# Kernel tuning notes

Hardware: AMD Instinct MI355X
Metric: run time of the kernel (lower is better)

Reference implementation:

```python
import jax, jax.numpy as jnp
import numpy as np

N = 8192        # agents (single node type VEHICLE)
K = 15          # max_Nnode - 1 neighbors per node
E = N * K       # edges
FT = 12         # prediction horizon steps
SD = 4          # state dim (x, y, vx, vy)
ID = 2          # input dim (ax, ay)
ZD = 8          # latent z dim
HE = 256        # history_enc_dim
EE = 128        # edge_enc_dim
OH = 256        # obs_lstm_hidden_dim
GH = 256        # guide_RNN_hidden_dim
FH = 256        # FC_hidden_dim
AD = 16         # att_internal_dim
DT = 0.25
SCALE = 1.0     # input_scale


def setup_inputs() -> dict:
    ks = jax.random.split(jax.random.key(0), 40)
    f = lambda i, s: jax.random.normal(ks[i], s, jnp.float32)
    w = lambda i, s: 0.05 * jax.random.normal(ks[i], s, jnp.float32)
    inp = dict(
        x_last=f(0, (N, SD)), x_st_last=f(1, (N, SD)), hist_enc=f(2, (N, HE)),
        z=f(3, (N, ZD)),
        node_size=jax.random.uniform(ks[4], (N, 2), jnp.float32, 1.0, 3.0),
        W_h0=w(5, (SD, OH)), b_h0=w(6, (OH,)), W_c0=w(7, (SD, OH)), b_c0=w(8, (OH,)),
        W_gh=w(9, (HE + ZD, GH)), b_gh=w(10, (GH,)),
        W_gru_ih=w(11, (HE + ZD, 3 * GH)), W_gru_hh=w(12, (GH, 3 * GH)),
        b_gru_ih=w(13, (3 * GH,)), b_gru_hh=w(14, (3 * GH,)),
        W_proj=w(15, (GH, 2)), b_proj=w(16, (2,)),
        W_att1=w(17, (EE, AD)), W_att2=w(18, (SD, AD)), v_att=w(19, (AD,)),
        W_lstm_ih=w(20, (EE, 4 * OH)), W_lstm_hh=w(21, (OH, 4 * OH)),
        b_lstm_ih=w(22, (4 * OH,)), b_lstm_hh=w(23, (4 * OH,)),
        W_e1=w(24, (SD + 4, FH)), b_e1=w(25, (FH,)), W_e2=w(26, (FH, EE)), b_e2=w(27, (EE,)),
        W_a1=w(28, (OH + ZD + SD + 4, FH)), b_a1=w(29, (FH,)),
        W_a2=w(30, (FH, ID)), b_a2=w(31, (ID,)),
    )
    # edge k is the j-th neighbor of node k // K; index 0 in the enc table is the pad row
    inp["edge_idx1"] = jnp.repeat(jnp.arange(N), K)
    inp["edge_idx2"] = jax.random.randint(ks[32], (E,), 0, N)
    inp["node_obs_idx"] = (jnp.arange(E) + 1).reshape(N, K)
    inp["ft"] = FT
    return inp


def _dyn(s, u):
    # double-integrator: s = [x, y, vx, vy], u = [ax, ay]
    pos = s[:, :2] + s[:, 2:4] * DT + 0.5 * u * DT * DT
    vel = s[:, 2:4] + u * DT
    return jnp.concatenate([pos, vel], -1)


def _forward(x_last, x_st_last, hist_enc, z, node_size,
             W_h0, b_h0, W_c0, b_c0, W_gh, b_gh, W_gru_ih, W_gru_hh, b_gru_ih, b_gru_hh,
             W_proj, b_proj, W_att1, W_att2, v_att, W_lstm_ih, W_lstm_hh, b_lstm_ih, b_lstm_hh,
             W_e1, b_e1, W_e2, b_e2, W_a1, b_a1, W_a2, b_a2,
             edge_idx1, edge_idx2, node_obs_idx, ft):
    n = x_last.shape[0]
    ee = W_e2.shape[1]
    # ---- guide GRU: desired trajectory [ft, N, 2] ----
    xz = jnp.concatenate([hist_enc, z], -1)
    h0g = xz @ W_gh + b_gh
    gi = xz @ W_gru_ih + b_gru_ih  # input is constant over time (xz repeated)
    ir, iz, inn = jnp.split(gi, 3, -1)

    def gru_step(h, _):
        hr, hz, hn = jnp.split(h @ W_gru_hh + b_gru_hh, 3, -1)
        r = jax.nn.sigmoid(ir + hr)
        u = jax.nn.sigmoid(iz + hz)
        nh = (1.0 - u) * jnp.tanh(inn + r * hn) + u * h
        return nh, nh

    _, hs = jax.lax.scan(gru_step, h0g, None, length=ft)
    des = hs @ W_proj + b_proj                       # [ft, N, 2]
    des_next = jnp.concatenate([des[1:], des[-1:]], 0)
    des_prev = jnp.concatenate([jnp.zeros_like(des[:1]), des[:-1]], 0)
    first = jnp.zeros((ft,), jnp.float32).at[0].set(1.0)

    # ---- obs LSTM initial state ----
    h0 = x_st_last @ W_h0 + b_h0
    c0 = x_st_last @ W_c0 + b_c0

    size1 = node_size[edge_idx1]
    size2 = node_size[edge_idx2]
    rad = 0.5 * (jnp.linalg.norm(size1, axis=-1) + jnp.linalg.norm(size2, axis=-1))

    def step(carry, xs):
        prev, prev_st, h, c, terr, ccost = carry
        des_t, des_n, des_p, fst = xs
        # edge gather + collision cost + edge encoding
        s1 = prev[edge_idx1]
        s2 = prev[edge_idx2]
        dist = jnp.linalg.norm(s1[:, :2] - s2[:, :2], axis=-1)
        ccost = ccost + jnp.sum(jax.nn.relu(rad - dist))
        feat = jnp.concatenate([s2 - s1, size1, size2], -1)          # [E, SD+4]
        enc = jax.nn.relu(feat @ W_e1 + b_e1) @ W_e2 + b_e2          # [E, EE]
        enc_all = jnp.concatenate([jnp.zeros((1, ee), enc.dtype), enc], 0)
        obs = enc_all[node_obs_idx]                                   # [N, K, EE]
        # relative state (t==0 uses standardized history directly)
        m = 1.0 - fst
        rel = prev_st - m * x_st_last
        rel = jnp.concatenate([rel[:, :2] - m * des_p, rel[:, 2:]], -1)
        terr = terr + jnp.linalg.norm(rel[:, :2]) / n
        next_wp = des_t - prev_st[:, :2]
        next_wp2 = des_n - prev_st[:, :2]
        # additive attention over neighbors
        scores = jnp.tanh(obs @ W_att1 + (rel @ W_att2)[:, None, :]) @ v_att   # [N, K]
        att = jax.nn.softmax(scores, axis=-1)
        ctx = jnp.einsum('nk,nkd->nd', att, obs)
        # LSTM cell (torch gate order i, f, g, o)
        gates = ctx @ W_lstm_ih + b_lstm_ih + h @ W_lstm_hh + b_lstm_hh
        g_i, g_f, g_g, g_o = jnp.split(gates, 4, -1)
        c = jax.nn.sigmoid(g_f) * c + jax.nn.sigmoid(g_i) * jnp.tanh(g_g)
        h = jax.nn.sigmoid(g_o) * jnp.tanh(c)
        # action net + dynamics rollout
        a_in = jnp.concatenate([h, z, rel, next_wp, next_wp2], -1)   # [N, OH+ZD+SD+4]
        u = SCALE * jnp.tanh(jax.nn.relu(a_in @ W_a1 + b_a1) @ W_a2 + b_a2)
        nxt = _dyn(prev, u)
        nxt_st = _dyn(prev_st, u)
        return (nxt, nxt_st, h, c, terr, ccost), (nxt, u)

    zero = jnp.zeros((), jnp.float32)
    init = (x_last, x_st_last, h0, c0, zero, zero)
    (_, _, _, _, terr, ccost), (state_pred, input_pred) = jax.lax.scan(
        step, init, (des, des_next, des_prev, first))
    return state_pred, input_pred, terr, ccost


def reference(x_last, x_st_last, hist_enc, z, node_size,
              W_h0, b_h0, W_c0, b_c0, W_gh, b_gh, W_gru_ih, W_gru_hh, b_gru_ih, b_gru_hh,
              W_proj, b_proj, W_att1, W_att2, v_att, W_lstm_ih, W_lstm_hh, b_lstm_ih, b_lstm_hh,
              W_e1, b_e1, W_e2, b_e2, W_a1, b_a1, W_a2, b_a2,
              edge_idx1, edge_idx2, node_obs_idx, ft):
    return _forward(x_last, x_st_last, hist_enc, z, node_size,
                    W_h0, b_h0, W_c0, b_c0, W_gh, b_gh, W_gru_ih, W_gru_hh, b_gru_ih, b_gru_hh,
                    W_proj, b_proj, W_att1, W_att2, v_att, W_lstm_ih, W_lstm_hh, b_lstm_ih, b_lstm_hh,
                    W_e1, b_e1, W_e2, b_e2, W_a1, b_a1, W_a2, b_a2,
                    edge_idx1, edge_idx2, node_obs_idx, ft)
```

## Files before the change

### kernel.cpp

```cpp
#include <hip/hip_runtime.h>

#define DEVI __device__ __forceinline__

constexpr int N_  = 8192;
constexpr int K_  = 15;
constexpr int E_  = N_ * K_;
constexpr int FTS = 12;
constexpr float DT_ = 0.25f;

typedef __attribute__((ext_vector_type(8))) short short8x;
typedef __attribute__((ext_vector_type(4))) float float4x;

union U8 { unsigned int u[4]; short8x v; };

DEVI float sigf(float x) { return 1.0f / (1.0f + __expf(-x)); }
DEVI float tanhf_fast(float x) { float e = __expf(2.f * x); return 1.f - 2.f / (e + 1.f); }
DEVI unsigned int f2u(float x) { union { float f; unsigned int u; } c; c.f = x; return c.u; }
DEVI float u2f(unsigned int x) { union { unsigned int u; float f; } c; c.u = x; return c.f; }

DEVI void split8(const float* __restrict__ s, short8x& hi8, short8x& lo8) {
  U8 ph, pl;
#pragma unroll
  for (int p = 0; p < 4; p++) {
    float a0 = s[2*p], a1 = s[2*p+1];
    unsigned int u0 = f2u(a0), u1 = f2u(a1);
    unsigned int h0 = u0 & 0xFFFF0000u, h1 = u1 & 0xFFFF0000u;
    ph.u[p] = (u0 >> 16) | h1;
    float l0 = a0 - u2f(h0), l1 = a1 - u2f(h1);
    pl.u[p] = (f2u(l0) >> 16) | (f2u(l1) & 0xFFFF0000u);
  }
  hi8 = ph.v; lo8 = pl.v;
}

__global__ void k_zero(float* ss) {
  ss[blockIdx.x * 256 + threadIdx.x] = 0.f;
}

__global__ __launch_bounds__(256) void k_edge_static(
    const int* __restrict__ e1, const int* __restrict__ e2,
    const float* __restrict__ nsize, float* __restrict__ rad, float* __restrict__ szf)
{
  int e = blockIdx.x * 256 + threadIdx.x;
  if (e >= E_) return;
  int i1 = e1[e], i2 = e2[e];
  float s1x = nsize[i1*2+0], s1y = nsize[i1*2+1];
  float s2x = nsize[i2*2+0], s2y = nsize[i2*2+1];
  rad[e] = 0.5f * (sqrtf(s1x*s1x + s1y*s1y) + sqrtf(s2x*s2x + s2y*s2y));
  *(float4*)&szf[e*4] = make_float4(s1x, s1y, s2x, s2y);
}

__global__ __launch_bounds__(256) void k_prep_hi(
    const float* __restrict__ W, unsigned short* __restrict__ out)
{
  int t = blockIdx.x * 256 + threadIdx.x;
  int fid = t >> 6, L = t & 63;
  int ks = fid >> 3, nt = fid & 7;
  int k0 = ks * 32 + (L >> 4) * 8;
  int n  = nt * 16 + (L & 15);
  unsigned int hi[4];
#pragma unroll
  for (int p = 0; p < 4; p++) {
    float w0 = W[(size_t)(k0 + 2*p) * 128 + n];
    float w1 = W[(size_t)(k0 + 2*p + 1) * 128 + n];
    hi[p] = (f2u(w0) >> 16) | (f2u(w1) & 0xFFFF0000u);
  }
  *(uint4*)(out + (size_t)fid * 512 + (size_t)L * 8) = make_uint4(hi[0], hi[1], hi[2], hi[3]);
}

__global__ __launch_bounds__(256) void k_prep1(
    const float* __restrict__ WA, const float* __restrict__ WB,
    int mode, int split, int wA, int wB, int Ktot, int NT, int nfrag,
    unsigned short* __restrict__ out)
{
  int t = blockIdx.x * 256 + threadIdx.x;
  int fid = t >> 6, L = t & 63;
  if (fid >= nfrag) return;
  int ks = fid / NT, nt = fid % NT;
  int k0 = ks * 32 + (L >> 4) * 8;
  int n  = nt * 16 + (L & 15);
  unsigned int hi[4];
#pragma unroll
  for (int p = 0; p < 4; p++) {
    float w0 = 0.f, w1 = 0.f;
    int ka = k0 + 2*p, kb = ka + 1;
    if (mode == 0) {
      if (ka < Ktot) w0 = (ka < split) ? WA[(size_t)ka*wA + n] : WB[(size_t)(ka-split)*wB + n];
      if (kb < Ktot) w1 = (kb < split) ? WA[(size_t)kb*wA + n] : WB[(size_t)(kb-split)*wB + n];
    } else {
      if (ka < Ktot) w0 = (n < split) ? WA[(size_t)ka*wA + n] : WB[(size_t)ka*wB + (n-split)];
      if (kb < Ktot) w1 = (n < split) ? WA[(size_t)kb*wA + n] : WB[(size_t)kb*wB + (n-split)];
    }
    hi[p] = (f2u(w0) >> 16) | (f2u(w1) & 0xFFFF0000u);
  }
  *(uint4*)(out + (size_t)fid * 512 + (size_t)L * 8) = make_uint4(hi[0], hi[1], hi[2], hi[3]);
}

__global__ __launch_bounds__(256) void k_xz_mfma(
    const float* __restrict__ hist, const float* __restrict__ z,
    const unsigned short* __restrict__ wB,
    const float* __restrict__ b_gh, const float* __restrict__ b_gih,
    float* __restrict__ gh0, unsigned int* __restrict__ gi_ru,
    float* __restrict__ gi_n)
{
  __shared__ __align__(16) float Abuf[2][64][36];
  const int tid = threadIdx.x;
  const int w = tid >> 6, lane = tid & 63;
  const int m = lane & 15, q = lane >> 4;
  const int n0 = blockIdx.x * 64;
  const int r_ = tid >> 2, c_ = (tid & 3) * 8;
  float4x acc[16];
#pragma unroll
  for (int tl = 0; tl < 16; tl++) acc[tl] = (float4x){0.f,0.f,0.f,0.f};

  auto LD = [&](int ks, float4& v0, float4& v1) {
    int kk = ks*32 + c_;
    int n = n0 + r_;
    if (kk < 256) {
      v0 = *(const float4*)&hist[(size_t)n*256 + kk];
      v1 = *(const float4*)&hist[(size_t)n*256 + kk + 4];
    } else if (kk == 256) {
      v0 = *(const float4*)&z[n*8];
      v1 = *(const float4*)&z[n*8 + 4];
    } else {
      v0 = make_float4(0,0,0,0); v1 = v0;
    }
  };
  {
    float4 v0, v1; LD(0, v0, v1);
    *(float4*)&Abuf[0][r_][c_]     = v0;
    *(float4*)&Abuf[0][r_][c_ + 4] = v1;
  }
  __syncthreads();
  for (int ks = 0; ks < 9; ks++) {
    float4 v0, v1;
    if (ks < 8) LD(ks + 1, v0, v1);
    short8x aHi, aLo;
    split8(&Abuf[ks & 1][w*16 + m][q*8], aHi, aLo);
#pragma unroll
    for (int tl = 0; tl < 16; tl++) {
      int nt = blockIdx.y*16 + tl;
      size_t off = (size_t)(ks*64 + nt) * 512 + (size_t)lane*8;
      short8x bh = *(const short8x*)(wB + off);
      acc[tl] = __builtin_amdgcn_mfma_f32_16x16x32_bf16(aLo, bh, acc[tl], 0, 0, 0);
      acc[tl] = __builtin_amdgcn_mfma_f32_16x16x32_bf16(aHi, bh, acc[tl], 0, 0, 0);
    }
    if (ks < 8) {
      *(float4*)&Abuf[(ks+1) & 1][r_][c_]     = v0;
      *(float4*)&Abuf[(ks+1) & 1][r_][c_ + 4] = v1;
      __syncthreads();
    }
  }
#pragma unroll
  for (int tl = 0; tl < 16; tl++) {
    int col = (blockIdx.y*16 + tl)*16 + m;
    float bias = (col < 256) ? b_gh[col] : b_gih[col - 256];
#pragma unroll
    for (int i = 0; i < 4; i++) {
      int n = n0 + w*16 + q*4 + i;
      float v = acc[tl][i] + bias;
      if (col < 256) {
        gh0[(size_t)n*256 + col] = v;
      } else {
        int cj = col - 256;
        int gate = cj >> 8, j = cj & 255;
        if (gate == 2) gi_n[(size_t)n*256 + j] = v;
        else ((unsigned short*)gi_ru)[((size_t)n*256 + j)*2 + gate] =
               (unsigned short)(f2u(v) >> 16);
      }
    }
  }
}

__global__ __launch_bounds__(512) void k_gru_all(
    const float* __restrict__ gh0, const unsigned short* __restrict__ wB,
    const float* __restrict__ b_ghh,
    const unsigned int* __restrict__ gi_ru, const float* __restrict__ gi_n,
    const float* __restrict__ W_proj, const float* __restrict__ b_proj,
    float* __restrict__ des)
{
  __shared__ __align__(16) float h_lds[2][32][260];
  __shared__ float sm_des[4][32][2];
  const int tid = threadIdx.x;
  const int w = tid >> 6, lane = tid & 63;
  const int m = lane & 15, q = lane >> 4;
  const int rh = w & 1, jh = w >> 1;
  const int n0 = blockIdx.x * 32;

  {
    int r = tid >> 4, c = (tid & 15) * 16;
    const float4* src = (const float4*)&gh0[(size_t)(n0 + r)*256 + c];
    float4 v0 = src[0], v1 = src[1], v2 = src[2], v3 = src[3];
    *(float4*)&h_lds[0][r][c]      = v0;
    *(float4*)&h_lds[0][r][c + 4]  = v1;
    *(float4*)&h_lds[0][r][c + 8]  = v2;
    *(float4*)&h_lds[0][r][c + 12] = v3;
  }
  float br_[4], bz_[4], bn_[4], wp0_[4], wp1_[4];
#pragma unroll
  for (int jt = 0; jt < 4; jt++) {
    int j = jh*64 + jt*16 + m;
    br_[jt] = b_ghh[j];
    bz_[jt] = b_ghh[256 + j];
    bn_[jt] = b_ghh[512 + j];
    wp0_[jt] = W_proj[j*2];
    wp1_[jt] = W_proj[j*2 + 1];
  }
  const float bp0 = b_proj[0], bp1 = b_proj[1];
  __syncthreads();

  for (int t = 0; t < FTS; t++) {
    float (*hc)[260] = h_lds[t & 1];
    float (*hn)[260] = h_lds[(t + 1) & 1];
    float4x acc[12];
#pragma unroll
    for (int tl = 0; tl < 12; tl++) acc[tl] = (float4x){0.f,0.f,0.f,0.f};

#pragma unroll 2
    for (int ks = 0; ks < 8; ks++) {
      float a8[8];
      {
        const float* hp = &hc[rh*16 + m][ks*32 + q*8];
        float4 v0 = *(const float4*)hp;
        float4 v1 = *(const float4*)(hp + 4);
        a8[0]=v0.x; a8[1]=v0.y; a8[2]=v0.z; a8[3]=v0.w;
        a8[4]=v1.x; a8[5]=v1.y; a8[6]=v1.z; a8[7]=v1.w;
      }
      short8x aHi, aLo;
      split8(a8, aHi, aLo);
#pragma unroll
      for (int tl = 0; tl < 12; tl++) {
        int g = tl >> 2, jt = tl & 3;
        int nt = g*16 + jh*4 + jt;
        size_t off = (size_t)(ks*48 + nt) * 512 + (size_t)lane*8;
        short8x bh = *(const short8x*)(wB + off);
        acc[tl] = __builtin_amdgcn_mfma_f32_16x16x32_bf16(aLo, bh, acc[tl], 0, 0, 0);
        acc[tl] = __builtin_amdgcn_mfma_f32_16x16x32_bf16(aHi, bh, acc[tl], 0, 0, 0);
      }
    }
    float pd0[4] = {0,0,0,0}, pd1[4] = {0,0,0,0};
#pragma unroll
    for (int jt = 0; jt < 4; jt++) {
      int j = jh*64 + jt*16 + m;
#pragma unroll
      for (int i = 0; i < 4; i++) {
        int rl = rh*16 + q*4 + i;
        unsigned int ru = gi_ru[(size_t)(n0 + rl)*256 + j];
        float ir  = u2f(ru << 16);
        float iz  = u2f(ru & 0xFFFF0000u);
        float inn = gi_n[(size_t)(n0 + rl)*256 + j];
        float hold = hc[rl][j];
        float r = sigf(ir + acc[0*4 + jt][i] + br_[jt]);
        float u = sigf(iz + acc[1*4 + jt][i] + bz_[jt]);
        float nh = (1.f - u) * tanhf_fast(inn + r * (acc[2*4 + jt][i] + bn_[jt])) + u * hold;
        hn[rl][j] = nh;
        pd0[i] += nh * wp0_[jt];
        pd1[i] += nh * wp1_[jt];
      }
    }
#pragma unroll
    for (int off = 1; off < 16; off <<= 1) {
#pragma unroll
      for (int i = 0; i < 4; i++) {
        pd0[i] += __shfl_xor(pd0[i], off);
        pd1[i] += __shfl_xor(pd1[i], off);
      }
    }
    if (m == 0) {
#pragma unroll
      for (int i = 0; i < 4; i++) {
        sm_des[jh][rh*16 + q*4 + i][0] = pd0[i];
        sm_des[jh][rh*16 + q*4 + i][1] = pd1[i];
      }
    }
    __syncthreads();
    if (tid < 64) {
      int r = tid >> 1, c = tid & 1;
      float s = sm_des[0][r][c] + sm_des[1][r][c] + sm_des[2][r][c] + sm_des[3][r][c];
      des[((size_t)t * N_ + n0 + r) * 2 + c] = s + (c ? bp1 : bp0);
    }
    __syncthreads();
  }
}

__global__ __launch_bounds__(256) void k_lstm_mfma(
    const float* __restrict__ ctxg, const float* __restrict__ h_in,
    const unsigned short* __restrict__ wB,
    const float* __restrict__ b_ih, const float* __restrict__ b_hh,
    float* __restrict__ c_st, float* __restrict__ h_out)
{
  __shared__ __align__(16) float Abuf[2][64][36];
  const int tid = threadIdx.x;
  const int w = tid >> 6, lane = tid & 63;
  const int m = lane & 15, q = lane >> 4;
  const int n0 = blockIdx.x * 64;
  const int j0 = blockIdx.y * 32;
  const int r_ = tid >> 2, c_ = (tid & 3) * 8;
  float4x acc[8];
#pragma unroll
  for (int tl = 0; tl < 8; tl++) acc[tl] = (float4x){0.f,0.f,0.f,0.f};

  auto LD = [&](int ks, float4& v0, float4& v1) {
    int kk = ks*32 + c_;
    int n = n0 + r_;
    if (kk < 128) {
      v0 = *(const float4*)&ctxg[(size_t)n*128 + kk];
      v1 = *(const float4*)&ctxg[(size_t)n*128 + kk + 4];
    } else {
      v0 = *(const float4*)&h_in[(size_t)n*256 + kk - 128];
      v1 = *(const float4*)&h_in[(size_t)n*256 + kk - 124];
    }
  };
  {
    float4 v0, v1; LD(0, v0, v1);
    *(float4*)&Abuf[0][r_][c_]     = v0;
    *(float4*)&Abuf[0][r_][c_ + 4] = v1;
  }
  __syncthreads();
  for (int ks = 0; ks < 12; ks++) {
    float4 v0, v1;
    if (ks < 11) LD(ks + 1, v0, v1);
    short8x aHi, aLo;
    split8(&Abuf[ks & 1][w*16 + m][q*8], aHi, aLo);
#pragma unroll
    for (int tl = 0; tl < 8; tl++) {
      int g = tl >> 1, jt = tl & 1;
      int nt = g*16 + (j0 >> 4) + jt;
      size_t off = (size_t)(ks*64 + nt) * 512 + (size_t)lane*8;
      short8x bh = *(const short8x*)(wB + off);
      acc[tl] = __builtin_amdgcn_mfma_f32_16x16x32_bf16(aLo, bh, acc[tl], 0, 0, 0);
      acc[tl] = __builtin_amdgcn_mfma_f32_16x16x32_bf16(aHi, bh, acc[tl], 0, 0, 0);
    }
    if (ks < 11) {
      *(float4*)&Abuf[(ks+1) & 1][r_][c_]     = v0;
      *(float4*)&Abuf[(ks+1) & 1][r_][c_ + 4] = v1;
      __syncthreads();
    }
  }
#pragma unroll
  for (int jt = 0; jt < 2; jt++) {
    int j = j0 + jt*16 + m;
    float bi = b_ih[j]       + b_hh[j];
    float bf = b_ih[256 + j] + b_hh[256 + j];
    float bg = b_ih[512 + j] + b_hh[512 + j];
    float bo = b_ih[768 + j] + b_hh[768 + j];
#pragma unroll
    for (int i = 0; i < 4; i++) {
      int n = n0 + w*16 + q*4 + i;
      float g_i = sigf(acc[0*2 + jt][i] + bi);
      float g_f = sigf(acc[1*2 + jt][i] + bf);
      float g_g = tanhf_fast(acc[2*2 + jt][i] + bg);
      float g_o = sigf(acc[3*2 + jt][i] + bo);
      float cv = g_f * c_st[(size_t)n*256 + j] + g_i * g_g;
      c_st[(size_t)n*256 + j] = cv;
      h_out[(size_t)n*256 + j] = g_o * tanhf_fast(cv);
    }
  }
}

__global__ __launch_bounds__(256) void k_action_mfma(
    const float* __restrict__ h, const float* __restrict__ z,
    const float* __restrict__ rel, const float* __restrict__ nwp, const float* __restrict__ nwp2,
    const unsigned short* __restrict__ wB, const float* __restrict__ b_a1,
    const float* __restrict__ W_a2, const float* __restrict__ b_a2,
    float* __restrict__ prev, float* __restrict__ prev_st,
    float* __restrict__ outS, float* __restrict__ outU)
{
  __shared__ __align__(16) float Abuf[2][32][36];
  __shared__ float sm_p[2][16][2];
  const int tid = threadIdx.x;
  const int w = tid >> 6, lane = tid & 63;
  const int m = lane & 15, q = lane >> 4;
  const int ng = w >> 1, hh = w & 1;
  const int n0 = blockIdx.x * 32;
  const int r_ = tid >> 3, c_ = (tid & 7) * 4;
  float4x acc[8];
#pragma unroll
  for (int j = 0; j < 8; j++) acc[j] = (float4x){0.f,0.f,0.f,0.f};

  auto LD = [&](int ks) -> float4 {
    int kk = ks*32 + c_;
    int n = n0 + r_;
    float4 v;
    if (kk < 256)       v = *(const float4*)&h[(size_t)n*256 + kk];
    else if (kk == 256) v = *(const float4*)&z[n*8];
    else if (kk == 260) v = *(const float4*)&z[n*8 + 4];
    else if (kk == 264) v = *(const float4*)&rel[n*4];
    else if (kk == 268) {
      float2 w1 = *(const float2*)&nwp[n*2];
      float2 w2 = *(const float2*)&nwp2[n*2];
      v = make_float4(w1.x, w1.y, w2.x, w2.y);
    } else v = make_float4(0,0,0,0);
    return v;
  };
  {
    float4 v = LD(0);
    *(float4*)&Abuf[0][r_][c_] = v;
  }
  __syncthreads();
  for (int ks = 0; ks < 9; ks++) {
    float4 v;
    if (ks < 8) v = LD(ks + 1);
    short8x aHi, aLo;
    split8(&Abuf[ks & 1][ng*16 + m][q*8], aHi, aLo);
#pragma unroll
    for (int j = 0; j < 8; j++) {
      int tl = hh*8 + j;
      size_t off = (size_t)(ks*16 + tl) * 512 + (size_t)lane*8;
      short8x bh = *(const short8x*)(wB + off);
      acc[j] = __builtin_amdgcn_mfma_f32_16x16x32_bf16(aLo, bh, acc[j], 0, 0, 0);
      acc[j] = __builtin_amdgcn_mfma_f32_16x16x32_bf16(aHi, bh, acc[j], 0, 0, 0);
    }
    if (ks < 8) {
      *(float4*)&Abuf[(ks+1) & 1][r_][c_] = v;
      __syncthreads();
    }
  }
  float p0[4] = {0,0,0,0}, p1[4] = {0,0,0,0};
#pragma unroll
  for (int j = 0; j < 8; j++) {
    int col = (hh*8 + j)*16 + m;
    float ba = b_a1[col];
    float2 w2 = *(const float2*)&W_a2[col*2];
#pragma unroll
    for (int i = 0; i < 4; i++) {
      float hv = fmaxf(acc[j][i] + ba, 0.f);
      p0[i] += hv * w2.x;
      p1[i] += hv * w2.y;
    }
  }
#pragma unroll
  for (int off = 1; off < 16; off <<= 1) {
#pragma unroll
    for (int i = 0; i < 4; i++) {
      p0[i] += __shfl_xor(p0[i], off);
      p1[i] += __shfl_xor(p1[i], off);
    }
  }
  if (hh == 1 && m == 0) {
#pragma unroll
    for (int i = 0; i < 4; i++) {
      sm_p[ng][q*4 + i][0] = p0[i];
      sm_p[ng][q*4 + i][1] = p1[i];
    }
  }
  __syncthreads();
  if (hh == 0 && m == 0) {
    float ba0 = b_a2[0], ba1 = b_a2[1];
    const float hd = 0.5f * DT_ * DT_;
#pragma unroll
    for (int i = 0; i < 4; i++) {
      int n = n0 + ng*16 + q*4 + i;
      float ux = tanhf_fast(p0[i] + sm_p[ng][q*4 + i][0] + ba0);
      float uy = tanhf_fast(p1[i] + sm_p[ng][q*4 + i][1] + ba1);
      float4 pv = *(const float4*)&prev[n*4];
      float4 ps = *(const float4*)&prev_st[n*4];
      float4 npv, nps;
      npv.x = pv.x + pv.z*DT_ + ux*hd;
      npv.y = pv.y + pv.w*DT_ + uy*hd;
      npv.z = pv.z + ux*DT_;
      npv.w = pv.w + uy*DT_;
      nps.x = ps.x + ps.z*DT_ + ux*hd;
      nps.y = ps.y + ps.w*DT_ + uy*hd;
      nps.z = ps.z + ux*DT_;
      nps.w = ps.w + uy*DT_;
      *(float4*)&prev[n*4] = npv;
      *(float4*)&prev_st[n*4] = nps;
      *(float4*)&outS[(size_t)n*4] = npv;
      outU[n*2]     = ux;
      outU[n*2 + 1] = uy;
    }
  }
}

__global__ __launch_bounds__(256) void k_init_hc(
    const float* __restrict__ x_last, const float* __restrict__ x_st_last,
    const float* __restrict__ W_h0, const float* __restrict__ b_h0,
    const float* __restrict__ W_c0, const float* __restrict__ b_c0,
    float* __restrict__ h, float* __restrict__ c,
    float* __restrict__ prev, float* __restrict__ prev_st)
{
  const int n = blockIdx.x;
  const int j = threadIdx.x;
  float x0 = x_st_last[n*4], x1 = x_st_last[n*4+1], x2 = x_st_last[n*4+2], x3 = x_st_last[n*4+3];
  h[(size_t)n*256 + j] = b_h0[j] + x0*W_h0[j] + x1*W_h0[256+j] + x2*W_h0[512+j] + x3*W_h0[768+j];
  c[(size_t)n*256 + j] = b_c0[j] + x0*W_c0[j] + x1*W_c0[256+j] + x2*W_c0[512+j] + x3*W_c0[768+j];
  if (j < 4) prev[n*4 + j] = x_last[n*4 + j];
  else if (j < 8) prev_st[n*4 + (j-4)] = x_st_last[n*4 + (j-4)];
}

__global__ __launch_bounds__(256, 4) void k_edge(
    const float* __restrict__ prev, const float* __restrict__ prev_st,
    const float* __restrict__ x_st_last,
    const float* __restrict__ szf, const float* __restrict__ rad,
    const int* __restrict__ nobs, const int* __restrict__ e1, const int* __restrict__ e2,
    const float* __restrict__ W_e1, const float* __restrict__ b_e1,
    const unsigned short* __restrict__ wsB, const float* __restrict__ b_e2,
    const unsigned short* __restrict__ wattA, const float* __restrict__ W_att2,
    const float* __restrict__ v_att,
    const float* __restrict__ des_p, const float* __restrict__ des_t,
    const float* __restrict__ des_n,
    float* __restrict__ relg, float* __restrict__ nwp, float* __restrict__ nwp2,
    float* __restrict__ ctx, float* __restrict__ ss_t, float* __restrict__ cc)
{
  __shared__ __align__(16) float smem[4776];
  const int tid = threadIdx.x;
  const int eb = blockIdx.x;

  float* sm_stage = smem;
  float* sm_feats = smem + 4096;
  float* sm_flags = smem + 4608;
  float* sm_relv  = smem + 4672;
  float* sm_watt2 = smem + 4688;
  float* sm_vatt  = smem + 4752;
  float* sm_red   = smem + 4768;

  const int n0  = eb * 4;
  const int slot = (eb & 15) << 4;
  const int lane = tid & 63;
  const int g    = tid >> 6;
  const int q = lane >> 4, m = lane & 15;

  if (tid >= 176 && tid < 192) sm_vatt[tid - 176] = v_att[tid - 176];
  if (tid >= 192) sm_watt2[tid - 192] = W_att2[tid - 192];

  if (tid < 64) {
    float v = 0.f;
    if (tid < 60) {
      int gg = tid / 15, k = tid % 15;
      int idx = nobs[(n0 + gg) * 15 + k];
      float f[8] = {0,0,0,0,0,0,0,0};
      float fl = 0.f;
      if (idx > 0) {
        int e = idx - 1;
        int i1 = e1[e], i2 = e2[e];
#pragma unroll
        for (int d = 0; d < 4; d++) f[d] = prev[i2*4 + d] - prev[i1*4 + d];
        float4 sz = *(const float4*)&szf[(size_t)e*4];
        f[4] = sz.x; f[5] = sz.y; f[6] = sz.z; f[7] = sz.w;
        fl = 1.f;
        float dist = sqrtf(f[0]*f[0] + f[1]*f[1]);
        v = fmaxf(rad[e] - dist, 0.f);
      }
#pragma unroll
      for (int d = 0; d < 8; d++) sm_feats[(gg*16 + k)*8 + d] = f[d];
      sm_flags[gg*16 + k] = fl;
    } else {
      int gg = tid - 60;
#pragma unroll
      for (int d = 0; d < 8; d++) sm_feats[(gg*16 + 15)*8 + d] = 0.f;
      sm_flags[gg*16 + 15] = 0.f;
    }
#pragma unroll
    for (int off = 32; off; off >>= 1) v += __shfl_down(v, off);
    if (tid == 0) atomicAdd(cc + slot, v);
  } else if (tid < 68) {
    int gg = tid - 64;
    int n = n0 + gg;
    float4 ps = *(const float4*)&prev_st[n*4];
    float r0, r1, r2, r3;
    if (des_p) {
      float4 xs = *(const float4*)&x_st_last[n*4];
      r0 = ps.x - xs.x - des_p[n*2];
      r1 = ps.y - xs.y - des_p[n*2 + 1];
      r2 = ps.z - xs.z;
      r3 = ps.w - xs.w;
    } else { r0 = ps.x; r1 = ps.y; r2 = ps.z; r3 = ps.w; }
    sm_relv[gg*4+0] = r0; sm_relv[gg*4+1] = r1; sm_relv[gg*4+2] = r2; sm_relv[gg*4+3] = r3;
    *(float4*)&relg[n*4] = make_float4(r0, r1, r2, r3);
    nwp[n*2]      = des_t[n*2]     - ps.x;
    nwp[n*2 + 1]  = des_t[n*2 + 1] - ps.y;
    nwp2[n*2]     = des_n[n*2]     - ps.x;
    nwp2[n*2 + 1] = des_n[n*2 + 1] - ps.y;
    sm_red[gg] = r0*r0 + r1*r1;
  }
  {
    const uint4* src = (const uint4*)wsB;
    uint4* dst = (uint4*)sm_stage;
    dst[tid]       = src[tid];
    dst[tid + 256] = src[tid + 256];
  }
  __syncthreads();
  if (tid == 64) atomicAdd(ss_t + slot, sm_red[0] + sm_red[1] + sm_red[2] + sm_red[3]);

  float f[8];
  {
    const float4 fa = *(const float4*)&sm_feats[(g*16 + m)*8];
    const float4 fb = *(const float4*)&sm_feats[(g*16 + m)*8 + 4];
    f[0]=fa.x; f[1]=fa.y; f[2]=fa.z; f[3]=fa.w; f[4]=fb.x; f[5]=fb.y; f[6]=fb.z; f[7]=fb.w;
  }
  float4x encR[8];
#pragma unroll
  for (int nt = 0; nt < 8; nt++) encR[nt] = (float4x){0.f,0.f,0.f,0.f};
  const float4* We14 = (const float4*)W_e1;
  const float4* Be14 = (const float4*)b_e1;

  for (int ks = 0; ks < 8; ks++) {
    uint4 r0, r1;
    if (ks < 7) {
      const uint4* src = (const uint4*)wsB + (ks + 1) * 512;
      r0 = src[tid];
      r1 = src[tid + 256];
    }
    short8x aHi, aLo;
    {
      float h8[8];
      float4 b0 = Be14[8*ks + 2*q];
      float4 b1 = Be14[8*ks + 2*q + 1];
      h8[0]=b0.x; h8[1]=b0.y; h8[2]=b0.z; h8[3]=b0.w; h8[4]=b1.x; h8[5]=b1.y; h8[6]=b1.z; h8[7]=b1.w;
#pragma unroll
      for (int d = 0; d < 8; d++) {
        float4 wa = We14[d*64 + ks*8 + 2*q];
        float4 wb = We14[d*64 + ks*8 + 2*q + 1];
        h8[0] += f[d]*wa.x; h8[1] += f[d]*wa.y; h8[2] += f[d]*wa.z; h8[3] += f[d]*wa.w;
        h8[4] += f[d]*wb.x; h8[5] += f[d]*wb.y; h8[6] += f[d]*wb.z; h8[7] += f[d]*wb.w;
      }
#pragma unroll
      for (int p = 0; p < 8; p++) h8[p] = fmaxf(h8[p], 0.f);
      split8(h8, aHi, aLo);
    }
    const unsigned short* sb = (const unsigned short*)sm_stage + (ks & 1) * 4096;
#pragma unroll
    for (int nt = 0; nt < 8; nt++) {
      short8x bh = *(const short8x*)(sb + nt*512 + lane*8);
      encR[nt] = __builtin_amdgcn_mfma_f32_16x16x32_bf16(aLo, bh, encR[nt], 0, 0, 0);
      encR[nt] = __builtin_amdgcn_mfma_f32_16x16x32_bf16(aHi, bh, encR[nt], 0, 0, 0);
    }
    if (ks < 7) {
      uint4* dst = (uint4*)sm_stage + ((ks + 1) & 1) * 512;
      dst[tid]       = r0;
      dst[tid + 256] = r1;
      __syncthreads();
    }
  }
  float4x fl4 = *(const float4x*)&sm_flags[g*16 + q*4];
#pragma unroll
  for (int nt = 0; nt < 8; nt++) {
    float b2 = b_e2[nt*16 + m];
#pragma unroll
    for (int i = 0; i < 4; i++) encR[nt][i] = (encR[nt][i] + b2) * fl4[i];
  }

  __syncthreads();
  {
  }
  float* tb = sm_stage + g * 576;
  float4x sacc = {0.f, 0.f, 0.f, 0.f};
#pragma unroll
  for (int ksc = 0; ksc < 4; ksc++) {
#pragma unroll
    for (int ntl = 0; ntl < 2; ntl++) {
#pragma unroll
      for (int i = 0; i < 4; i++)
        tb[(q*4 + i)*36 + ntl*16 + m] = encR[2*ksc + ntl][i];
    }
    __builtin_amdgcn_s_waitcnt(0);
    float a8[8];
    {
      const float4* tp = (const float4*)(tb + m*36 + q*8);
      float4 t0 = tp[0], t1 = tp[1];
      a8[0]=t0.x; a8[1]=t0.y; a8[2]=t0.z; a8[3]=t0.w;
      a8[4]=t1.x; a8[5]=t1.y; a8[6]=t1.z; a8[7]=t1.w;
    }
    __builtin_amdgcn_s_waitcnt(0);
    short8x aH, aL;
    split8(a8, aH, aL);
    short8x bh = *(const short8x*)(wattA + ksc*512 + lane*8);
    sacc = __builtin_amdgcn_mfma_f32_16x16x32_bf16(aL, bh, sacc, 0, 0, 0);
    sacc = __builtin_amdgcn_mfma_f32_16x16x32_bf16(aH, bh, sacc, 0, 0, 0);
  }

  float relw;
  {
    float4 rv = *(const float4*)&sm_relv[g*4];
    relw = rv.x * sm_watt2[m] + rv.y * sm_watt2[16 + m]
         + rv.z * sm_watt2[32 + m] + rv.w * sm_watt2[48 + m];
  }
  float vat = sm_vatt[m];
  float val[4];
#pragma unroll
  for (int i = 0; i < 4; i++) val[i] = tanhf_fast(sacc[i] + relw) * vat;
#pragma unroll
  for (int msk = 1; msk < 16; msk <<= 1) {
#pragma unroll
    for (int i = 0; i < 4; i++) val[i] += __shfl_xor(val[i], msk);
  }
  if (q == 3) val[3] = -3.0e38f;
  float mx = fmaxf(fmaxf(val[0], val[1]), fmaxf(val[2], val[3]));
  mx = fmaxf(mx, __shfl_xor(mx, 16));
  mx = fmaxf(mx, __shfl_xor(mx, 32));
  float4x ev;
  float ssum = 0.f;
#pragma unroll
  for (int i = 0; i < 4; i++) { ev[i] = __expf(val[i] - mx); ssum += ev[i]; }
  ssum += __shfl_xor(ssum, 16);
  ssum += __shfl_xor(ssum, 32);
  float inv = 1.f / ssum;
#pragma unroll
  for (int i = 0; i < 4; i++) ev[i] *= inv;

  float cpart[8];
#pragma unroll
  for (int nt = 0; nt < 8; nt++) {
    float cv = ev[0]*encR[nt][0] + ev[1]*encR[nt][1] + ev[2]*encR[nt][2] + ev[3]*encR[nt][3];
    cv += __shfl_xor(cv, 16);
    cv += __shfl_xor(cv, 32);
    cpart[nt] = cv;
  }
  float v0 = (q == 0) ? cpart[0] : (q == 1) ? cpart[2] : (q == 2) ? cpart[4] : cpart[6];
  float v1 = (q == 0) ? cpart[1] : (q == 1) ? cpart[3] : (q == 2) ? cpart[5] : cpart[7];
  size_t cb = (size_t)(n0 + g) * 128 + q*32 + m;
  ctx[cb]      = v0;
  ctx[cb + 16] = v1;
}

__global__ void k_final(const float* __restrict__ ss, float* __restrict__ out) {
  const int lane = threadIdx.x;
  float red[13];
#pragma unroll
  for (int a = 0; a < 13; a++) {
    float v = (lane < 16) ? ss[a*256 + lane*16] : 0.f;
    v += __shfl_xor(v, 1);
    v += __shfl_xor(v, 2);
    v += __shfl_xor(v, 4);
    v += __shfl_xor(v, 8);
    red[a] = v;
  }
  if (lane == 0) {
    float t = 0.f;
    for (int i = 0; i < FTS; i++) t += sqrtf(red[i]);
    out[(size_t)FTS * N_ * 6]     = t / (float)N_;
    out[(size_t)FTS * N_ * 6 + 1] = red[12];
  }
}

extern "C" void kernel_launch(void* const* d_in, const int* in_sizes, int n_in,
                              void* d_out, int out_size, void* d_ws, size_t ws_size,
                              hipStream_t stream) {
  (void)in_sizes; (void)n_in; (void)out_size; (void)ws_size;
  const float* x_last    = (const float*)d_in[0];
  const float* x_st_last = (const float*)d_in[1];
  const float* hist_enc  = (const float*)d_in[2];
  const float* z         = (const float*)d_in[3];
  const float* node_size = (const float*)d_in[4];
  const float* W_h0 = (const float*)d_in[5];
  const float* b_h0 = (const float*)d_in[6];
  const float* W_c0 = (const float*)d_in[7];
  const float* b_c0 = (const float*)d_in[8];
  const float* W_gh = (const float*)d_in[9];
  const float* b_gh = (const float*)d_in[10];
  const float* W_gih = (const float*)d_in[11];
  const float* W_ghh = (const float*)d_in[12];
  const float* b_gih = (const float*)d_in[13];
  const float* b_ghh = (const float*)d_in[14];
  const float* W_proj = (const float*)d_in[15];
  const float* b_proj = (const float*)d_in[16];
  const float* W_att1 = (const float*)d_in[17];
  const float* W_att2 = (const float*)d_in[18];
  const float* v_att  = (const float*)d_in[19];
  const float* W_lih = (const float*)d_in[20];
  const float* W_lhh = (const float*)d_in[21];
  const float* b_lih = (const float*)d_in[22];
  const float* b_lhh = (const float*)d_in[23];
  const float* W_e1 = (const float*)d_in[24];
  const float* b_e1 = (const float*)d_in[25];
  const float* W_e2 = (const float*)d_in[26];
  const float* b_e2 = (const float*)d_in[27];
  const float* W_a1 = (const float*)d_in[28];
  const float* b_a1 = (const float*)d_in[29];
  const float* W_a2 = (const float*)d_in[30];
  const float* b_a2 = (const float*)d_in[31];
  const int* e1   = (const int*)d_in[32];
  const int* e2   = (const int*)d_in[33];
  const int* nobs = (const int*)d_in[34];
  float* out = (float*)d_out;

  float* wsf     = (float*)d_ws;
  float* prev    = wsf;
  float* prev_st = wsf + 32768;
  float* des     = wsf + 65536;
  float* rad     = wsf + 262160;
  float* szf     = wsf + 385040;
  float* baseA   = wsf + 876560;
  float* gh0           = baseA;
  unsigned int* gi_ru  = (unsigned int*)(baseA + (size_t)2 * N_ * 256);
  float* gi_n          = baseA + (size_t)3 * N_ * 256;
  float* hA   = baseA;
  float* hB   = baseA + (size_t)N_ * 256;
  float* cbuf = baseA + (size_t)2 * N_ * 256;
  float* ctx  = baseA + (size_t)3 * N_ * 256;
  float* rel  = baseA + (size_t)4 * N_ * 256;
  float* nwp  = rel + (size_t)N_ * 4;
  float* nwp2 = nwp + (size_t)N_ * 2;
  unsigned short* wsBe = (unsigned short*)(wsf + 11362320);
  unsigned short* wsBg = (unsigned short*)(wsf + 11427856);
  unsigned short* wsBl = (unsigned short*)(wsf + 11624464);
  unsigned short* wsBx = (unsigned short*)(wsf + 12017680);
  unsigned short* wsBa = (unsigned short*)(wsf + 12312592);
  unsigned short* wattA = (unsigned short*)(wsf + 12386320);
  float* ssx = wsf + 12388368;

  k_zero<<<13, 256, 0, stream>>>(ssx);
  k_edge_static<<<(E_ + 255) / 256, 256, 0, stream>>>(e1, e2, node_size, rad, szf);

  k_prep_hi<<<16, 256, 0, stream>>>(W_e2, wsBe);
  k_prep1<<<96,  256, 0, stream>>>(W_ghh, W_ghh, 0, 256, 768,  768,  256, 48, 384, wsBg);
  k_prep1<<<192, 256, 0, stream>>>(W_lih, W_lhh, 0, 128, 1024, 1024, 384, 64, 768, wsBl);
  k_prep1<<<144, 256, 0, stream>>>(W_gh,  W_gih, 1, 256, 256,  768,  264, 64, 576, wsBx);
  k_prep1<<<36,  256, 0, stream>>>(W_a1,  W_a1,  0, 272, 256,  256,  272, 16, 144, wsBa);
  k_prep1<<<1,   256, 0, stream>>>(W_att1, W_att1, 0, 128, 16, 16, 128, 1, 4, wattA);

  k_xz_mfma<<<dim3(128, 4), 256, 0, stream>>>(hist_enc, z, wsBx, b_gh, b_gih,
                                              gh0, gi_ru, gi_n);
  k_gru_all<<<256, 512, 0, stream>>>(gh0, wsBg, b_ghh, gi_ru, gi_n,
                                     W_proj, b_proj, des);

  k_init_hc<<<N_, 256, 0, stream>>>(x_last, x_st_last, W_h0, b_h0, W_c0, b_c0,
                                    hA, cbuf, prev, prev_st);
  float* hcur = hA;
  float* hnxt = hB;
  for (int t = 0; t < FTS; t++) {
    const float* des_t = des + (size_t)t * N_ * 2;
    const float* des_n = des + (size_t)((t + 1 < FTS) ? t + 1 : FTS - 1) * N_ * 2;
    const float* des_p = (t > 0) ? des + (size_t)(t - 1) * N_ * 2 : nullptr;
    k_edge<<<2048, 256, 0, stream>>>(prev, prev_st, x_st_last, szf, rad,
                                     nobs, e1, e2, W_e1, b_e1, wsBe, b_e2,
                                     wattA, W_att2, v_att,
                                     des_p, des_t, des_n,
                                     rel, nwp, nwp2, ctx,
                                     ssx + (size_t)t * 256, ssx + 12 * 256);
    k_lstm_mfma<<<dim3(128, 8), 256, 0, stream>>>(ctx, hcur, wsBl, b_lih, b_lhh,
                                                  cbuf, hnxt);
    k_action_mfma<<<256, 256, 0, stream>>>(hnxt, z, rel, nwp, nwp2,
                                           wsBa, b_a1, W_a2, b_a2,
                                           prev, prev_st,
                                           out + (size_t)t * N_ * 4,
                                           out + (size_t)FTS * N_ * 4 + (size_t)t * N_ * 2);
    float* tmp = hcur; hcur = hnxt; hnxt = tmp;
  }
  k_final<<<1, 64, 0, stream>>>(ssx, out);
}
```

Measured before the change: 1.479 ms.

## Prefetch GRU weights into registers, hoist gate inputs, single-buffer hidden state

```diff
diff --git a/kernel.cpp b/kernel.cpp
--- a/kernel.cpp
+++ b/kernel.cpp
@@ -171,14 +171,14 @@
   }
 }
 
-__global__ __launch_bounds__(512) void k_gru_all(
+__global__ __launch_bounds__(512, 2) void k_gru_all(
     const float* __restrict__ gh0, const unsigned short* __restrict__ wB,
     const float* __restrict__ b_ghh,
     const unsigned int* __restrict__ gi_ru, const float* __restrict__ gi_n,
     const float* __restrict__ W_proj, const float* __restrict__ b_proj,
     float* __restrict__ des)
 {
-  __shared__ __align__(16) float h_lds[2][32][260];
+  __shared__ __align__(16) float h_lds[32][260];
   __shared__ float sm_des[4][32][2];
   const int tid = threadIdx.x;
   const int w = tid >> 6, lane = tid & 63;
@@ -190,10 +190,10 @@
     int r = tid >> 4, c = (tid & 15) * 16;
     const float4* src = (const float4*)&gh0[(size_t)(n0 + r)*256 + c];
     float4 v0 = src[0], v1 = src[1], v2 = src[2], v3 = src[3];
-    *(float4*)&h_lds[0][r][c]      = v0;
-    *(float4*)&h_lds[0][r][c + 4]  = v1;
-    *(float4*)&h_lds[0][r][c + 8]  = v2;
-    *(float4*)&h_lds[0][r][c + 12] = v3;
+    *(float4*)&h_lds[r][c]      = v0;
+    *(float4*)&h_lds[r][c + 4]  = v1;
+    *(float4*)&h_lds[r][c + 8]  = v2;
+    *(float4*)&h_lds[r][c + 12] = v3;
   }
   float br_[4], bz_[4], bn_[4], wp0_[4], wp1_[4];
 #pragma unroll
@@ -206,20 +206,48 @@
     wp1_[jt] = W_proj[j*2 + 1];
   }
   const float bp0 = b_proj[0], bp1 = b_proj[1];
+  float ir_[4][4], iz_[4][4], inn_[4][4];
+#pragma unroll
+  for (int jt = 0; jt < 4; jt++) {
+    int j = jh*64 + jt*16 + m;
+#pragma unroll
+    for (int i = 0; i < 4; i++) {
+      int rl = rh*16 + q*4 + i;
+      unsigned int ru = gi_ru[(size_t)(n0 + rl)*256 + j];
+      ir_[jt][i]  = u2f(ru << 16);
+      iz_[jt][i]  = u2f(ru & 0xFFFF0000u);
+      inn_[jt][i] = gi_n[(size_t)(n0 + rl)*256 + j];
+    }
+  }
+  const unsigned short* __restrict__ wLane = wB + (size_t)lane * 8;
   __syncthreads();
 
+#pragma unroll 1
   for (int t = 0; t < FTS; t++) {
-    float (*hc)[260] = h_lds[t & 1];
-    float (*hn)[260] = h_lds[(t + 1) & 1];
     float4x acc[12];
 #pragma unroll
     for (int tl = 0; tl < 12; tl++) acc[tl] = (float4x){0.f,0.f,0.f,0.f};
 
-#pragma unroll 2
+    short8x bcur[12], bnxt[12];
+#pragma unroll
+    for (int tl = 0; tl < 12; tl++) {
+      int g = tl >> 2, jt = tl & 3;
+      int nt = g*16 + jh*4 + jt;
+      bcur[tl] = *(const short8x*)(wLane + (size_t)nt * 512);
+    }
+#pragma unroll
     for (int ks = 0; ks < 8; ks++) {
+      if (ks < 7) {
+#pragma unroll
+        for (int tl = 0; tl < 12; tl++) {
+          int g = tl >> 2, jt = tl & 3;
+          int nt = g*16 + jh*4 + jt;
+          bnxt[tl] = *(const short8x*)(wLane + (size_t)((ks + 1)*48 + nt) * 512);
+        }
+      }
       float a8[8];
       {
-        const float* hp = &hc[rh*16 + m][ks*32 + q*8];
+        const float* hp = &h_lds[rh*16 + m][ks*32 + q*8];
         float4 v0 = *(const float4*)hp;
         float4 v1 = *(const float4*)(hp + 4);
         a8[0]=v0.x; a8[1]=v0.y; a8[2]=v0.z; a8[3]=v0.w;
@@ -229,14 +257,13 @@
       split8(a8, aHi, aLo);
 #pragma unroll
       for (int tl = 0; tl < 12; tl++) {
-        int g = tl >> 2, jt = tl & 3;
-        int nt = g*16 + jh*4 + jt;
-        size_t off = (size_t)(ks*48 + nt) * 512 + (size_t)lane*8;
-        short8x bh = *(const short8x*)(wB + off);
-        acc[tl] = __builtin_amdgcn_mfma_f32_16x16x32_bf16(aLo, bh, acc[tl], 0, 0, 0);
-        acc[tl] = __builtin_amdgcn_mfma_f32_16x16x32_bf16(aHi, bh, acc[tl], 0, 0, 0);
+        acc[tl] = __builtin_amdgcn_mfma_f32_16x16x32_bf16(aLo, bcur[tl], acc[tl], 0, 0, 0);
+        acc[tl] = __builtin_amdgcn_mfma_f32_16x16x32_bf16(aHi, bcur[tl], acc[tl], 0, 0, 0);
       }
-    }
+#pragma unroll
+      for (int tl = 0; tl < 12; tl++) bcur[tl] = bnxt[tl];
+    }
+    __syncthreads();
     float pd0[4] = {0,0,0,0}, pd1[4] = {0,0,0,0};
 #pragma unroll
     for (int jt = 0; jt < 4; jt++) {
@@ -244,15 +271,11 @@
 #pragma unroll
       for (int i = 0; i < 4; i++) {
         int rl = rh*16 + q*4 + i;
-        unsigned int ru = gi_ru[(size_t)(n0 + rl)*256 + j];
-        float ir  = u2f(ru << 16);
-        float iz  = u2f(ru & 0xFFFF0000u);
-        float inn = gi_n[(size_t)(n0 + rl)*256 + j];
-        float hold = hc[rl][j];
-        float r = sigf(ir + acc[0*4 + jt][i] + br_[jt]);
-        float u = sigf(iz + acc[1*4 + jt][i] + bz_[jt]);
-        float nh = (1.f - u) * tanhf_fast(inn + r * (acc[2*4 + jt][i] + bn_[jt])) + u * hold;
-        hn[rl][j] = nh;
+        float hold = h_lds[rl][j];
+        float r = sigf(ir_[jt][i] + acc[0*4 + jt][i] + br_[jt]);
+        float u = sigf(iz_[jt][i] + acc[1*4 + jt][i] + bz_[jt]);
+        float nh = (1.f - u) * tanhf_fast(inn_[jt][i] + r * (acc[2*4 + jt][i] + bn_[jt])) + u * hold;
+        h_lds[rl][j] = nh;
         pd0[i] += nh * wp0_[jt];
         pd1[i] += nh * wp1_[jt];
       }
@@ -278,7 +301,6 @@
       float s = sm_des[0][r][c] + sm_des[1][r][c] + sm_des[2][r][c] + sm_des[3][r][c];
       des[((size_t)t * N_ + n0 + r) * 2 + c] = s + (c ? bp1 : bp0);
     }
-    __syncthreads();
   }
 }
 
```

New measurement: 1.777 ms. 20.1% more time.
